# Kernel optimization log

Measured on AMD Instinct MI355X. Metric: run time of the kernel, lower is better.

The kernel has to match this reference:

```python
import jax, jax.numpy as jnp
import numpy as np

B, S, D, H = 4, 2048, 1024, 16
DH = D // H
NEG = -1.0e9


def setup_inputs() -> dict:
    key = jax.random.key(0)
    ks = jax.random.split(key, 12)
    sc = 1.0 / np.sqrt(D)
    inp = {
        'q': jax.random.normal(ks[0], (B, S, D), jnp.float32),
        'k': jax.random.normal(ks[1], (B, S, D), jnp.float32),
        'v': jax.random.normal(ks[2], (B, S, D), jnp.float32),
        # causal mask: 1.0 where attention is disallowed (strictly upper triangular)
        'mask': jnp.triu(jnp.ones((S, S), jnp.float32), k=1)[None, None, :, :],
        'Wq': jax.random.normal(ks[3], (D, D), jnp.float32) * sc,
        'bq': jnp.zeros((D,), jnp.float32),
        'Wk': jax.random.normal(ks[4], (D, D), jnp.float32) * sc,
        'bk': jnp.zeros((D,), jnp.float32),
        'Wv': jax.random.normal(ks[5], (D, D), jnp.float32) * sc,
        'bv': jnp.zeros((D,), jnp.float32),
        'Wo': jax.random.normal(ks[6], (D, D), jnp.float32) * sc,
        'bo': jnp.zeros((D,), jnp.float32),
    }
    return inp


def _split_heads(x):
    # [B,S,D] -> [B,H,S,DH]
    return x.reshape(B, S, H, DH).transpose(0, 2, 1, 3)


def reference(q, k, v, mask, Wq, bq, Wk, bk, Wv, bv, Wo, bo):
    _q = _split_heads(q @ Wq.T + bq)
    _k = _split_heads(k @ Wk.T + bk)
    _v = _split_heads(v @ Wv.T + bv)
    # faithful quirk: mask*-1e9 added BEFORE scaling, scale = sqrt(model_dim)
    score = jnp.einsum('bhqd,bhkd->bhqk', _q, _k) + mask * NEG
    attn = jax.nn.softmax(score / jnp.sqrt(jnp.float32(D)), axis=-1)
    ctx = jnp.einsum('bhqk,bhkd->bhqd', attn, _v)
    ctx = ctx.transpose(0, 2, 1, 3).reshape(B, S, D)
    return ctx @ Wo.T + bo
```

## Files before the change

### kernel.cpp

```cpp
#include <hip/hip_runtime.h>
#include <hip/hip_bf16.h>

#define S_ 2048
#define DH_ 64
#define NE_ 8388608

using f32x4  = __attribute__((ext_vector_type(4))) float;
using bf16x8 = __attribute__((ext_vector_type(8))) __bf16;
using bf16x4 = __attribute__((ext_vector_type(4))) __bf16;

__device__ __forceinline__ unsigned int f2bf(float f) {
    union { float f; unsigned int u; } x; x.f = f;
    return (x.u + 0x7FFFu + ((x.u >> 16) & 1u)) >> 16;
}

__device__ __forceinline__ void gl_lds16(const unsigned short* g, unsigned short* l) {
    __builtin_amdgcn_global_load_lds(
        (const __attribute__((address_space(1))) unsigned int*)(const void*)g,
        (__attribute__((address_space(3))) unsigned int*)(void*)l,
        16, 0, 0);
}

__global__ __launch_bounds__(256) void cvt_w4(const float* __restrict__ w0, const float* __restrict__ w1,
                                              const float* __restrict__ w2, const float* __restrict__ w3,
                                              unsigned short* __restrict__ out) {
    const float* src = blockIdx.y == 0 ? w0 : blockIdx.y == 1 ? w1 : blockIdx.y == 2 ? w2 : w3;
    unsigned short* dst = out + (size_t)blockIdx.y * 1048576;
    int i = (blockIdx.x * 256 + threadIdx.x) * 4;
    float4 v = *(const float4*)&src[i];
    ushort4 h;
    h.x = f2bf(v.x); h.y = f2bf(v.y); h.z = f2bf(v.z); h.w = f2bf(v.w);
    *(ushort4*)&dst[i] = h;
}

__global__ __launch_bounds__(256) void cvt_a3(const float* __restrict__ a0, const float* __restrict__ a1,
                                              const float* __restrict__ a2, unsigned short* __restrict__ out) {
    const float* src = blockIdx.y == 0 ? a0 : blockIdx.y == 1 ? a1 : a2;
    unsigned short* dst = out + (size_t)blockIdx.y * NE_;
    int i = (blockIdx.x * 256 + threadIdx.x) * 4;
    float4 v = *(const float4*)&src[i];
    ushort4 h;
    h.x = f2bf(v.x); h.y = f2bf(v.y); h.z = f2bf(v.z); h.w = f2bf(v.w);
    *(ushort4*)&dst[i] = h;
}

__global__ __launch_bounds__(256) void gemm_qkv(const unsigned short* __restrict__ actb,
                                                const unsigned short* __restrict__ Wcat,
                                                const float* __restrict__ bq,
                                                const float* __restrict__ bk,
                                                const float* __restrict__ bvv,
                                                unsigned short* __restrict__ Qp,
                                                unsigned short* __restrict__ Kp,
                                                unsigned short* __restrict__ VTp,
                                                float scq)
{
    constexpr int K = 1024, BK = 32;
    __shared__ unsigned short As[128 * BK];
    __shared__ unsigned short Bs[128 * BK];

    const int tid = threadIdx.x, lane = tid & 63, wid = tid >> 6;
    const int row0 = blockIdx.x * 128, col0 = blockIdx.y * 128;
    const int range = blockIdx.y >> 3;
    const unsigned short* A = actb + (size_t)range * NE_;
    const int wm = (wid >> 1) * 64, wn = (wid & 1) * 64;
    const int fr = lane & 15, fg = lane >> 4;

    f32x4 acc[4][4] = {};

    const int srow = wid * 16 + (lane >> 2);
    const int scol = (lane & 3) * 8;
    const size_t abase = (size_t)(row0 + srow) * K + scol;
    const size_t bbase = (size_t)(col0 + srow) * K + scol;
    unsigned short* lA0 = &As[srow * BK + scol];
    unsigned short* lA1 = &As[(srow + 64) * BK + scol];
    unsigned short* lB0 = &Bs[srow * BK + scol];
    unsigned short* lB1 = &Bs[(srow + 64) * BK + scol];

    for (int k0 = 0; k0 < K; k0 += BK) {
        gl_lds16(&A[abase + k0], lA0);
        gl_lds16(&A[abase + (size_t)64 * K + k0], lA1);
        gl_lds16(&Wcat[bbase + k0], lB0);
        gl_lds16(&Wcat[bbase + (size_t)64 * K + k0], lB1);
        __syncthreads();

        bf16x8 af[4], bfr[4];
        #pragma unroll
        for (int i = 0; i < 4; ++i) af[i] = *(const bf16x8*)&As[(wm + i * 16 + fr) * BK + fg * 8];
        #pragma unroll
        for (int i = 0; i < 4; ++i) bfr[i] = *(const bf16x8*)&Bs[(wn + i * 16 + fr) * BK + fg * 8];
        #pragma unroll
        for (int i = 0; i < 4; ++i)
            #pragma unroll
            for (int j = 0; j < 4; ++j)
                acc[i][j] = __builtin_amdgcn_mfma_f32_16x16x32_bf16(af[i], bfr[j], acc[i][j], 0, 0, 0);
        __syncthreads();
    }

    const float os = range == 0 ? scq : 1.0f;
    const float* bp = range == 0 ? bq : range == 1 ? bk : bvv;
    unsigned short* OP = range == 0 ? Qp : Kp;

    #pragma unroll
    for (int i = 0; i < 4; ++i) {
        #pragma unroll
        for (int j = 0; j < 4; ++j) {
            int colr = (col0 + wn + j * 16 + fr) & 1023;
            float bias = bp[colr];
            int h = colr >> 6, dh = colr & 63;
            if (range == 2) {
                int row = row0 + wm + i * 16 + fg * 4;
                int b = row >> 11, s = row & 2047;
                unsigned int w0 = f2bf(acc[i][j][0] + bias) | (f2bf(acc[i][j][1] + bias) << 16);
                unsigned int w1 = f2bf(acc[i][j][2] + bias) | (f2bf(acc[i][j][3] + bias) << 16);
                *(uint2*)&VTp[((size_t)((b << 4) + h) * 64 + dh) * 2048 + s] = make_uint2(w0, w1);
            } else {
                #pragma unroll
                for (int r = 0; r < 4; ++r) {
                    int row = row0 + wm + i * 16 + fg * 4 + r;
                    int b = row >> 11, s = row & 2047;
                    OP[((((b << 4) + h) * 2048 + s) << 6) + dh] =
                        (unsigned short)f2bf((acc[i][j][r] + bias) * os);
                }
            }
        }
    }
}

__global__ __launch_bounds__(256) void gemm_o(const unsigned short* __restrict__ A,
                                              const unsigned short* __restrict__ Bw,
                                              const float* __restrict__ bias,
                                              float* __restrict__ Cf)
{
    constexpr int K = 1024, BK = 32, N = 1024;
    __shared__ unsigned short As[128 * BK];
    __shared__ unsigned short Bs[128 * BK];

    const int tid = threadIdx.x, lane = tid & 63, wid = tid >> 6;
    const int row0 = blockIdx.x * 128, col0 = blockIdx.y * 128;
    const int wm = (wid >> 1) * 64, wn = (wid & 1) * 64;
    const int fr = lane & 15, fg = lane >> 4;

    f32x4 acc[4][4] = {};

    const int srow = wid * 16 + (lane >> 2);
    const int scol = (lane & 3) * 8;
    const size_t abase = (size_t)(row0 + srow) * K + scol;
    const size_t bbase = (size_t)(col0 + srow) * K + scol;
    unsigned short* lA0 = &As[srow * BK + scol];
    unsigned short* lA1 = &As[(srow + 64) * BK + scol];
    unsigned short* lB0 = &Bs[srow * BK + scol];
    unsigned short* lB1 = &Bs[(srow + 64) * BK + scol];

    for (int k0 = 0; k0 < K; k0 += BK) {
        gl_lds16(&A[abase + k0], lA0);
        gl_lds16(&A[abase + (size_t)64 * K + k0], lA1);
        gl_lds16(&Bw[bbase + k0], lB0);
        gl_lds16(&Bw[bbase + (size_t)64 * K + k0], lB1);
        __syncthreads();

        bf16x8 af[4], bfr[4];
        #pragma unroll
        for (int i = 0; i < 4; ++i) af[i] = *(const bf16x8*)&As[(wm + i * 16 + fr) * BK + fg * 8];
        #pragma unroll
        for (int i = 0; i < 4; ++i) bfr[i] = *(const bf16x8*)&Bs[(wn + i * 16 + fr) * BK + fg * 8];
        #pragma unroll
        for (int i = 0; i < 4; ++i)
            #pragma unroll
            for (int j = 0; j < 4; ++j)
                acc[i][j] = __builtin_amdgcn_mfma_f32_16x16x32_bf16(af[i], bfr[j], acc[i][j], 0, 0, 0);
        __syncthreads();
    }

    #pragma unroll
    for (int i = 0; i < 4; ++i) {
        #pragma unroll
        for (int j = 0; j < 4; ++j) {
            int col = col0 + wn + j * 16 + fr;
            float bv = bias[col];
            #pragma unroll
            for (int r = 0; r < 4; ++r) {
                int row = row0 + wm + i * 16 + fg * 4 + r;
                Cf[(size_t)row * N + col] = acc[i][j][r] + bv;
            }
        }
    }
}

__global__ __launch_bounds__(512, 4) void attn_fwd5(const unsigned short* __restrict__ Qp,
                                                    const unsigned short* __restrict__ Kp,
                                                    const unsigned short* __restrict__ VTg,
                                                    unsigned short* __restrict__ ctx)
{
    __shared__ unsigned short Ks[64][68];
    __shared__ unsigned short Vt[64][68];
    __shared__ unsigned short Ps[8][16][68];

    const int lin = blockIdx.x;
    const int xcd = lin & 7;
    const int w = lin >> 3;
    const int bh = xcd * 8 + (w & 7);
    const int j = 15 - (w >> 3);
    const int b = bh >> 4, h = bh & 15;
    const int tid = threadIdx.x, lane = tid & 63, wid = tid >> 6;
    const int fr = lane & 15, fg = lane >> 4;

    const unsigned short* Qh  = Qp  + (size_t)bh * (S_ * DH_);
    const unsigned short* Kh  = Kp  + (size_t)bh * (S_ * DH_);
    const unsigned short* VTh = VTg + (size_t)bh * (DH_ * S_);

    const int srow = tid >> 3;
    const int scol = (tid & 7) * 8;

    bf16x8 ones;
    #pragma unroll
    for (int i = 0; i < 8; ++i) ones[i] = (__bf16)1.0f;

    const int q0 = j * 128;
    const int ntiles = 2 * (j + 1);
    const int rbase = q0 + wid * 16;
    const int qg = rbase + fr;

    bf16x8 qf[2];
    #pragma unroll
    for (int ks = 0; ks < 2; ++ks)
        qf[ks] = *(const bf16x8*)&Qh[(size_t)qg * 64 + ks * 32 + 8 * fg];

    f32x4 oacc[4] = {};
    float m_run = -3.0e38f, l_run = 0.0f;

    int4 kreg = *(const int4*)&Kh[(size_t)srow * 64 + scol];
    int4 vreg = *(const int4*)&VTh[(size_t)srow * 2048 + scol];

    for (int kt = 0; kt < ntiles; ++kt) {
        const int kv0 = kt * 64;
        __syncthreads();
        *(int4*)&Ks[srow][scol] = kreg;
        *(int4*)&Vt[srow][scol] = vreg;
        if (kt + 1 < ntiles) {
            const int kv1 = kv0 + 64;
            kreg = *(const int4*)&Kh[(size_t)(kv1 + srow) * 64 + scol];
            vreg = *(const int4*)&VTh[(size_t)srow * 2048 + kv1 + scol];
        }
        __syncthreads();

        if (kv0 > rbase + 15) continue;

        f32x4 sacc[4] = {};
        #pragma unroll
        for (int nt = 0; nt < 4; ++nt)
            #pragma unroll
            for (int ks = 0; ks < 2; ++ks) {
                bf16x8 kf = *(const bf16x8*)&Ks[nt * 16 + fr][ks * 32 + 8 * fg];
                sacc[nt] = __builtin_amdgcn_mfma_f32_16x16x32_bf16(kf, qf[ks], sacc[nt], 0, 0, 0);
            }

        if (kv0 + 63 > rbase) {
            const int kbase = kv0 + fg * 4;
            #pragma unroll
            for (int nt = 0; nt < 4; ++nt)
                #pragma unroll
                for (int r = 0; r < 4; ++r)
                    if (kbase + nt * 16 + r > qg) sacc[nt][r] = -3.0e38f;
        }

        float vm = sacc[0][0];
        #pragma unroll
        for (int nt = 0; nt < 4; ++nt)
            #pragma unroll
            for (int r = 0; r < 4; ++r) vm = fmaxf(vm, sacc[nt][r]);
        vm = fmaxf(vm, __shfl_xor(vm, 16));
        vm = fmaxf(vm, __shfl_xor(vm, 32));

        if (!__all(vm - m_run <= 8.0f)) {
            const float mn = fmaxf(m_run, vm);
            const float alpha = exp2f(m_run - mn);
            m_run = mn;
            l_run *= alpha;
            #pragma unroll
            for (int dt = 0; dt < 4; ++dt)
                #pragma unroll
                for (int r = 0; r < 4; ++r) oacc[dt][r] *= alpha;
        }

        #pragma unroll
        for (int nt = 0; nt < 4; ++nt) {
            bf16x4 t;
            t[0] = (__bf16)exp2f(sacc[nt][0] - m_run);
            t[1] = (__bf16)exp2f(sacc[nt][1] - m_run);
            t[2] = (__bf16)exp2f(sacc[nt][2] - m_run);
            t[3] = (__bf16)exp2f(sacc[nt][3] - m_run);
            *(bf16x4*)&Ps[wid][fr][nt * 16 + fg * 4] = t;
        }
        asm volatile("s_waitcnt lgkmcnt(0)" ::: "memory");

        bf16x8 pb[2];
        #pragma unroll
        for (int ks = 0; ks < 2; ++ks)
            pb[ks] = *(const bf16x8*)&Ps[wid][fr][ks * 32 + 8 * fg];

        f32x4 racc = {};
        #pragma unroll
        for (int ks = 0; ks < 2; ++ks)
            racc = __builtin_amdgcn_mfma_f32_16x16x32_bf16(ones, pb[ks], racc, 0, 0, 0);
        #pragma unroll
        for (int dt = 0; dt < 4; ++dt)
            #pragma unroll
            for (int ks = 0; ks < 2; ++ks) {
                bf16x8 vf = *(const bf16x8*)&Vt[dt * 16 + fr][ks * 32 + 8 * fg];
                oacc[dt] = __builtin_amdgcn_mfma_f32_16x16x32_bf16(vf, pb[ks], oacc[dt], 0, 0, 0);
            }
        l_run += racc[0];
    }

    const float linv = 1.0f / l_run;
    unsigned short* cb = &ctx[(size_t)(b * 2048 + qg) * 1024 + h * 64];
    #pragma unroll
    for (int dt = 0; dt < 4; ++dt) {
        unsigned int w0 = f2bf(oacc[dt][0] * linv) | (f2bf(oacc[dt][1] * linv) << 16);
        unsigned int w1 = f2bf(oacc[dt][2] * linv) | (f2bf(oacc[dt][3] * linv) << 16);
        *(uint2*)&cb[dt * 16 + fg * 4] = make_uint2(w0, w1);
    }
}

extern "C" void kernel_launch(void* const* d_in, const int* in_sizes, int n_in,
                              void* d_out, int out_size, void* d_ws, size_t ws_size,
                              hipStream_t stream)
{
    const float* q  = (const float*)d_in[0];
    const float* k  = (const float*)d_in[1];
    const float* v  = (const float*)d_in[2];
    const float* Wq = (const float*)d_in[4];
    const float* bq = (const float*)d_in[5];
    const float* Wk = (const float*)d_in[6];
    const float* bk = (const float*)d_in[7];
    const float* Wv = (const float*)d_in[8];
    const float* bv = (const float*)d_in[9];
    const float* Wo = (const float*)d_in[10];
    const float* bo = (const float*)d_in[11];
    float* out = (float*)d_out;

    unsigned short* Wcat = (unsigned short*)d_ws;
    unsigned short* actb = Wcat + 4 * 1048576;
    unsigned short* Qp   = actb + 3 * (size_t)NE_;
    unsigned short* Kp   = Qp + NE_;
    unsigned short* VTp  = Kp + NE_;
    unsigned short* Ctx  = VTp + NE_;

    const float SCQ = 0.045084220027780106f;

    dim3 blk(256);
    cvt_w4<<<dim3(1024, 4), blk, 0, stream>>>(Wq, Wk, Wv, Wo, Wcat);
    cvt_a3<<<dim3(8192, 3), blk, 0, stream>>>(q, k, v, actb);

    gemm_qkv<<<dim3(64, 24), blk, 0, stream>>>(actb, Wcat, bq, bk, bv, Qp, Kp, VTp, SCQ);

    attn_fwd5<<<dim3(1024), dim3(512), 0, stream>>>(Qp, Kp, VTp, Ctx);

    gemm_o<<<dim3(64, 8), blk, 0, stream>>>(Ctx, Wcat + 3 * 1048576, bo, out);
}
```

Before: 203.0 us.

## Fuse fp32-to-bf16 activation conversion into QKV GEMM and double-buffer GEMM tiles

Drops the separate activation conversion kernel. The QKV GEMM now loads fp32 q/k/v directly into registers, converts them to bf16 and writes them into a double-buffered LDS tile, prefetching the next tile while the current one is multiplied. The output projection GEMM also gets double-buffered LDS with async global-to-LDS prefetch. This removes an extra read/write pass over the activations and one launch, and overlaps loads with MFMA. In exchange the fp32 A reads are re-done by each column block (8 per range), LDS use doubles, and register pressure rises.

Measured after the change: 209.1 us. +3.0%, slower.

```diff
diff --git a/kernel.cpp b/kernel.cpp
--- a/kernel.cpp
+++ b/kernel.cpp
@@ -33,35 +33,26 @@
     *(ushort4*)&dst[i] = h;
 }
 
-__global__ __launch_bounds__(256) void cvt_a3(const float* __restrict__ a0, const float* __restrict__ a1,
-                                              const float* __restrict__ a2, unsigned short* __restrict__ out) {
-    const float* src = blockIdx.y == 0 ? a0 : blockIdx.y == 1 ? a1 : a2;
-    unsigned short* dst = out + (size_t)blockIdx.y * NE_;
-    int i = (blockIdx.x * 256 + threadIdx.x) * 4;
-    float4 v = *(const float4*)&src[i];
-    ushort4 h;
-    h.x = f2bf(v.x); h.y = f2bf(v.y); h.z = f2bf(v.z); h.w = f2bf(v.w);
-    *(ushort4*)&dst[i] = h;
-}
-
-__global__ __launch_bounds__(256) void gemm_qkv(const unsigned short* __restrict__ actb,
-                                                const unsigned short* __restrict__ Wcat,
-                                                const float* __restrict__ bq,
-                                                const float* __restrict__ bk,
-                                                const float* __restrict__ bvv,
-                                                unsigned short* __restrict__ Qp,
-                                                unsigned short* __restrict__ Kp,
-                                                unsigned short* __restrict__ VTp,
-                                                float scq)
+__global__ __launch_bounds__(256) void gemm_qkv_f(const float* __restrict__ qf32,
+                                                  const float* __restrict__ kf32,
+                                                  const float* __restrict__ vf32,
+                                                  const unsigned short* __restrict__ Wcat,
+                                                  const float* __restrict__ bq,
+                                                  const float* __restrict__ bk,
+                                                  const float* __restrict__ bvv,
+                                                  unsigned short* __restrict__ Qp,
+                                                  unsigned short* __restrict__ Kp,
+                                                  unsigned short* __restrict__ VTp,
+                                                  float scq)
 {
-    constexpr int K = 1024, BK = 32;
-    __shared__ unsigned short As[128 * BK];
-    __shared__ unsigned short Bs[128 * BK];
+    constexpr int K = 1024, BK = 32, NT = K / BK;
+    __shared__ unsigned short As[2][128 * BK];
+    __shared__ unsigned short Bs[2][128 * BK];
 
     const int tid = threadIdx.x, lane = tid & 63, wid = tid >> 6;
     const int row0 = blockIdx.x * 128, col0 = blockIdx.y * 128;
     const int range = blockIdx.y >> 3;
-    const unsigned short* A = actb + (size_t)range * NE_;
+    const float* A = range == 0 ? qf32 : range == 1 ? kf32 : vf32;
     const int wm = (wid >> 1) * 64, wn = (wid & 1) * 64;
     const int fr = lane & 15, fg = lane >> 4;
 
@@ -69,30 +60,61 @@
 
     const int srow = wid * 16 + (lane >> 2);
     const int scol = (lane & 3) * 8;
-    const size_t abase = (size_t)(row0 + srow) * K + scol;
     const size_t bbase = (size_t)(col0 + srow) * K + scol;
-    unsigned short* lA0 = &As[srow * BK + scol];
-    unsigned short* lA1 = &As[(srow + 64) * BK + scol];
-    unsigned short* lB0 = &Bs[srow * BK + scol];
-    unsigned short* lB1 = &Bs[(srow + 64) * BK + scol];
-
-    for (int k0 = 0; k0 < K; k0 += BK) {
-        gl_lds16(&A[abase + k0], lA0);
-        gl_lds16(&A[abase + (size_t)64 * K + k0], lA1);
-        gl_lds16(&Wcat[bbase + k0], lB0);
-        gl_lds16(&Wcat[bbase + (size_t)64 * K + k0], lB1);
-        __syncthreads();
+
+    const int arow = tid >> 1;
+    const int acol = (tid & 1) * 16;
+    const float* agp = A + (size_t)(row0 + arow) * K + acol;
+
+    float4 ar[4];
+    #pragma unroll
+    for (int u = 0; u < 4; ++u) ar[u] = *(const float4*)&agp[4 * u];
+
+    gl_lds16(&Wcat[bbase], &Bs[0][srow * BK + scol]);
+    gl_lds16(&Wcat[bbase + (size_t)64 * K], &Bs[0][(srow + 64) * BK + scol]);
+
+    {
+        bf16x8 h0, h1;
+        h0[0] = (__bf16)ar[0].x; h0[1] = (__bf16)ar[0].y; h0[2] = (__bf16)ar[0].z; h0[3] = (__bf16)ar[0].w;
+        h0[4] = (__bf16)ar[1].x; h0[5] = (__bf16)ar[1].y; h0[6] = (__bf16)ar[1].z; h0[7] = (__bf16)ar[1].w;
+        h1[0] = (__bf16)ar[2].x; h1[1] = (__bf16)ar[2].y; h1[2] = (__bf16)ar[2].z; h1[3] = (__bf16)ar[2].w;
+        h1[4] = (__bf16)ar[3].x; h1[5] = (__bf16)ar[3].y; h1[6] = (__bf16)ar[3].z; h1[7] = (__bf16)ar[3].w;
+        *(bf16x8*)&As[0][arow * BK + acol] = h0;
+        *(bf16x8*)&As[0][arow * BK + acol + 8] = h1;
+    }
+    __syncthreads();
+
+    for (int t = 0; t < NT; ++t) {
+        const int cur = t & 1;
+        const bool more = (t + 1 < NT);
+        if (more) {
+            const int k1 = (t + 1) * BK;
+            #pragma unroll
+            for (int u = 0; u < 4; ++u) ar[u] = *(const float4*)&agp[k1 + 4 * u];
+            gl_lds16(&Wcat[bbase + k1], &Bs[cur ^ 1][srow * BK + scol]);
+            gl_lds16(&Wcat[bbase + (size_t)64 * K + k1], &Bs[cur ^ 1][(srow + 64) * BK + scol]);
+        }
 
         bf16x8 af[4], bfr[4];
         #pragma unroll
-        for (int i = 0; i < 4; ++i) af[i] = *(const bf16x8*)&As[(wm + i * 16 + fr) * BK + fg * 8];
-        #pragma unroll
-        for (int i = 0; i < 4; ++i) bfr[i] = *(const bf16x8*)&Bs[(wn + i * 16 + fr) * BK + fg * 8];
+        for (int i = 0; i < 4; ++i) af[i] = *(const bf16x8*)&As[cur][(wm + i * 16 + fr) * BK + fg * 8];
+        #pragma unroll
+        for (int i = 0; i < 4; ++i) bfr[i] = *(const bf16x8*)&Bs[cur][(wn + i * 16 + fr) * BK + fg * 8];
         #pragma unroll
         for (int i = 0; i < 4; ++i)
             #pragma unroll
             for (int j = 0; j < 4; ++j)
                 acc[i][j] = __builtin_amdgcn_mfma_f32_16x16x32_bf16(af[i], bfr[j], acc[i][j], 0, 0, 0);
+
+        if (more) {
+            bf16x8 h0, h1;
+            h0[0] = (__bf16)ar[0].x; h0[1] = (__bf16)ar[0].y; h0[2] = (__bf16)ar[0].z; h0[3] = (__bf16)ar[0].w;
+            h0[4] = (__bf16)ar[1].x; h0[5] = (__bf16)ar[1].y; h0[6] = (__bf16)ar[1].z; h0[7] = (__bf16)ar[1].w;
+            h1[0] = (__bf16)ar[2].x; h1[1] = (__bf16)ar[2].y; h1[2] = (__bf16)ar[2].z; h1[3] = (__bf16)ar[2].w;
+            h1[4] = (__bf16)ar[3].x; h1[5] = (__bf16)ar[3].y; h1[6] = (__bf16)ar[3].z; h1[7] = (__bf16)ar[3].w;
+            *(bf16x8*)&As[cur ^ 1][arow * BK + acol] = h0;
+            *(bf16x8*)&As[cur ^ 1][arow * BK + acol + 8] = h1;
+        }
         __syncthreads();
     }
 
@@ -131,9 +153,9 @@
                                               const float* __restrict__ bias,
                                               float* __restrict__ Cf)
 {
-    constexpr int K = 1024, BK = 32, N = 1024;
-    __shared__ unsigned short As[128 * BK];
-    __shared__ unsigned short Bs[128 * BK];
+    constexpr int K = 1024, BK = 32, N = 1024, NT = K / BK;
+    __shared__ unsigned short As[2][128 * BK];
+    __shared__ unsigned short Bs[2][128 * BK];
 
     const int tid = threadIdx.x, lane = tid & 63, wid = tid >> 6;
     const int row0 = blockIdx.x * 128, col0 = blockIdx.y * 128;
@@ -146,23 +168,28 @@
     const int scol = (lane & 3) * 8;
     const size_t abase = (size_t)(row0 + srow) * K + scol;
     const size_t bbase = (size_t)(col0 + srow) * K + scol;
-    unsigned short* lA0 = &As[srow * BK + scol];
-    unsigned short* lA1 = &As[(srow + 64) * BK + scol];
-    unsigned short* lB0 = &Bs[srow * BK + scol];
-    unsigned short* lB1 = &Bs[(srow + 64) * BK + scol];
-
-    for (int k0 = 0; k0 < K; k0 += BK) {
-        gl_lds16(&A[abase + k0], lA0);
-        gl_lds16(&A[abase + (size_t)64 * K + k0], lA1);
-        gl_lds16(&Bw[bbase + k0], lB0);
-        gl_lds16(&Bw[bbase + (size_t)64 * K + k0], lB1);
-        __syncthreads();
+
+    gl_lds16(&A[abase], &As[0][srow * BK + scol]);
+    gl_lds16(&A[abase + (size_t)64 * K], &As[0][(srow + 64) * BK + scol]);
+    gl_lds16(&Bw[bbase], &Bs[0][srow * BK + scol]);
+    gl_lds16(&Bw[bbase + (size_t)64 * K], &Bs[0][(srow + 64) * BK + scol]);
+    __syncthreads();
+
+    for (int t = 0; t < NT; ++t) {
+        const int cur = t & 1;
+        if (t + 1 < NT) {
+            const int k1 = (t + 1) * BK;
+            gl_lds16(&A[abase + k1], &As[cur ^ 1][srow * BK + scol]);
+            gl_lds16(&A[abase + (size_t)64 * K + k1], &As[cur ^ 1][(srow + 64) * BK + scol]);
+            gl_lds16(&Bw[bbase + k1], &Bs[cur ^ 1][srow * BK + scol]);
+            gl_lds16(&Bw[bbase + (size_t)64 * K + k1], &Bs[cur ^ 1][(srow + 64) * BK + scol]);
+        }
 
         bf16x8 af[4], bfr[4];
         #pragma unroll
-        for (int i = 0; i < 4; ++i) af[i] = *(const bf16x8*)&As[(wm + i * 16 + fr) * BK + fg * 8];
-        #pragma unroll
-        for (int i = 0; i < 4; ++i) bfr[i] = *(const bf16x8*)&Bs[(wn + i * 16 + fr) * BK + fg * 8];
+        for (int i = 0; i < 4; ++i) af[i] = *(const bf16x8*)&As[cur][(wm + i * 16 + fr) * BK + fg * 8];
+        #pragma unroll
+        for (int i = 0; i < 4; ++i) bfr[i] = *(const bf16x8*)&Bs[cur][(wn + i * 16 + fr) * BK + fg * 8];
         #pragma unroll
         for (int i = 0; i < 4; ++i)
             #pragma unroll
@@ -340,8 +367,7 @@
     float* out = (float*)d_out;
 
     unsigned short* Wcat = (unsigned short*)d_ws;
-    unsigned short* actb = Wcat + 4 * 1048576;
-    unsigned short* Qp   = actb + 3 * (size_t)NE_;
+    unsigned short* Qp   = Wcat + 4 * 1048576;
     unsigned short* Kp   = Qp + NE_;
     unsigned short* VTp  = Kp + NE_;
     unsigned short* Ctx  = VTp + NE_;
@@ -350,9 +376,8 @@
 
     dim3 blk(256);
     cvt_w4<<<dim3(1024, 4), blk, 0, stream>>>(Wq, Wk, Wv, Wo, Wcat);
-    cvt_a3<<<dim3(8192, 3), blk, 0, stream>>>(q, k, v, actb);
-
-    gemm_qkv<<<dim3(64, 24), blk, 0, stream>>>(actb, Wcat, bq, bk, bv, Qp, Kp, VTp, SCQ);
+
+    gemm_qkv_f<<<dim3(64, 24), blk, 0, stream>>>(q, k, v, Wcat, bq, bk, bv, Qp, Kp, VTp, SCQ);
 
     attn_fwd5<<<dim3(1024), dim3(512), 0, stream>>>(Qp, Kp, VTp, Ctx);
 
```

## Rewrite QKV projection GEMM with 256x256 tiles, double-buffered LDS and swizzle

Applied to the files above, without the earlier changes.

Replaces the 128x128, 4-wave QKV GEMM with a 256x256-tile, 8-wave kernel that uses BK=64 and double-buffers A and B in LDS. Async global-to-LDS copies for the next k-tile are interleaved with the MFMA phases, using explicit waitcnt, barriers and setprio. An XOR swizzle is applied to LDS addresses, and blocks are remapped across XCDs so neighbouring tiles share cache. The aim is to raise arithmetic intensity and overlap memory latency with compute. The cost is 128 KB of LDS per block, more registers, and only 384 blocks, which lowers occupancy and parallelism.

Result: no change. 205.4 us (+1.2%).

```diff
diff --git a/kernel.cpp b/kernel.cpp
--- a/kernel.cpp
+++ b/kernel.cpp
@@ -44,71 +44,117 @@
     *(ushort4*)&dst[i] = h;
 }
 
-__global__ __launch_bounds__(256) void gemm_qkv(const unsigned short* __restrict__ actb,
-                                                const unsigned short* __restrict__ Wcat,
-                                                const float* __restrict__ bq,
-                                                const float* __restrict__ bk,
-                                                const float* __restrict__ bvv,
-                                                unsigned short* __restrict__ Qp,
-                                                unsigned short* __restrict__ Kp,
-                                                unsigned short* __restrict__ VTp,
-                                                float scq)
+__global__ __launch_bounds__(512, 2) void gemm_qkv8(const unsigned short* __restrict__ actb,
+                                                    const unsigned short* __restrict__ Wcat,
+                                                    const float* __restrict__ bq,
+                                                    const float* __restrict__ bk,
+                                                    const float* __restrict__ bvv,
+                                                    unsigned short* __restrict__ Qp,
+                                                    unsigned short* __restrict__ Kp,
+                                                    unsigned short* __restrict__ VTp,
+                                                    float scq)
 {
-    constexpr int K = 1024, BK = 32;
-    __shared__ unsigned short As[128 * BK];
-    __shared__ unsigned short Bs[128 * BK];
+    __shared__ unsigned short lds[65536];
+    unsigned short* ldsA = lds;
+    unsigned short* ldsB = lds + 32768;
+
+    const int orig = blockIdx.x;
+    const int lid = (orig & 7) * 48 + (orig >> 3);
+    const int bx = lid & 31;
+    const int by = lid >> 5;
+    const int range = by >> 2;
+    const unsigned short* Aact = actb + (size_t)range * NE_;
 
     const int tid = threadIdx.x, lane = tid & 63, wid = tid >> 6;
-    const int row0 = blockIdx.x * 128, col0 = blockIdx.y * 128;
-    const int range = blockIdx.y >> 3;
-    const unsigned short* A = actb + (size_t)range * NE_;
-    const int wm = (wid >> 1) * 64, wn = (wid & 1) * 64;
     const int fr = lane & 15, fg = lane >> 4;
-
-    f32x4 acc[4][4] = {};
-
-    const int srow = wid * 16 + (lane >> 2);
-    const int scol = (lane & 3) * 8;
-    const size_t abase = (size_t)(row0 + srow) * K + scol;
-    const size_t bbase = (size_t)(col0 + srow) * K + scol;
-    unsigned short* lA0 = &As[srow * BK + scol];
-    unsigned short* lA1 = &As[(srow + 64) * BK + scol];
-    unsigned short* lB0 = &Bs[srow * BK + scol];
-    unsigned short* lB1 = &Bs[(srow + 64) * BK + scol];
-
-    for (int k0 = 0; k0 < K; k0 += BK) {
-        gl_lds16(&A[abase + k0], lA0);
-        gl_lds16(&A[abase + (size_t)64 * K + k0], lA1);
-        gl_lds16(&Wcat[bbase + k0], lB0);
-        gl_lds16(&Wcat[bbase + (size_t)64 * K + k0], lB1);
-        __syncthreads();
-
-        bf16x8 af[4], bfr[4];
-        #pragma unroll
-        for (int i = 0; i < 4; ++i) af[i] = *(const bf16x8*)&As[(wm + i * 16 + fr) * BK + fg * 8];
-        #pragma unroll
-        for (int i = 0; i < 4; ++i) bfr[i] = *(const bf16x8*)&Bs[(wn + i * 16 + fr) * BK + fg * 8];
-        #pragma unroll
-        for (int i = 0; i < 4; ++i)
-            #pragma unroll
-            for (int j = 0; j < 4; ++j)
-                acc[i][j] = __builtin_amdgcn_mfma_f32_16x16x32_bf16(af[i], bfr[j], acc[i][j], 0, 0, 0);
-        __syncthreads();
-    }
-
+    const int wid_m = wid >> 2, wid_n = wid & 3;
+
+    const int srcRow0 = wid * 16 + (lane >> 3);
+    const int scolS = ((((lane & 7) * 16) ^ (lane & 32)) >> 1);
+
+    auto STG = [&](int ldsRegion, const unsigned short* g, int grow, int kk) {
+        const unsigned short* s0 = g + (size_t)(grow + srcRow0) * 1024 + kk + scolS;
+        gl_lds16(s0, lds + ldsRegion + wid * 1024 + lane * 8);
+        gl_lds16(s0 + 8 * 1024, lds + ldsRegion + wid * 1024 + 512 + lane * 8);
+    };
+
+    const int flipR = (fr & 4) ? 16 : 0;
+    const int vA = wid_m * 8192 + fr * 64 + ((fg * 8) ^ flipR);
+    const int vB = (wid_n & 1) * 4096 + fr * 64 + ((fg * 8) ^ flipR) + (wid_n >> 1) * 8192;
+
+    f32x4 acc[8][4] = {};
+    bf16x8 bfr[4][2];
+
+    STG(0,          Aact, bx * 256,       0);
+    STG(8192,       Aact, bx * 256 + 128, 0);
+    STG(32768,      Wcat, by * 256,       0);
+    STG(32768+8192, Wcat, by * 256 + 128, 0);
+    STG(32768+16384,       Wcat, by * 256,       64);
+    STG(32768+16384+8192,  Wcat, by * 256 + 128,  64);
+    asm volatile("s_waitcnt vmcnt(4)" ::: "memory");
+    __builtin_amdgcn_s_barrier();
+
+#define KTILE(BUF, ABUF, TA, BBUF, TB)                                              \
+  {                                                                                 \
+    _Pragma("unroll")                                                               \
+    for (int q = 0; q < 4; ++q) {                                                   \
+      if (q == 0) {                                                                 \
+        _Pragma("unroll")                                                           \
+        for (int j = 0; j < 4; ++j) {                                               \
+          bfr[j][0] = *(const bf16x8*)&ldsB[(BUF)*16384 + vB + j*1024];             \
+          bfr[j][1] = *(const bf16x8*)&ldsB[(BUF)*16384 + vB + j*1024 + 32];        \
+        }                                                                           \
+      }                                                                             \
+      bf16x8 af[2][2];                                                              \
+      _Pragma("unroll")                                                             \
+      for (int i2 = 0; i2 < 2; ++i2) {                                              \
+        af[i2][0] = *(const bf16x8*)&ldsA[(BUF)*16384 + vA + (q*2+i2)*1024];        \
+        af[i2][1] = *(const bf16x8*)&ldsA[(BUF)*16384 + vA + (q*2+i2)*1024 + 32];   \
+      }                                                                             \
+      if (q == 0) STG((ABUF)*16384,        Aact, bx*256,       ((TA)&15)*64);       \
+      if (q == 1) STG((ABUF)*16384 + 8192, Aact, bx*256 + 128, ((TA)&15)*64);       \
+      if (q == 2) STG(32768 + (BBUF)*16384,        Wcat, by*256,       ((TB)&15)*64); \
+      if (q == 3) { STG(32768 + (BBUF)*16384 + 8192, Wcat, by*256 + 128, ((TB)&15)*64); \
+                    asm volatile("s_waitcnt vmcnt(4)" ::: "memory"); }              \
+      __builtin_amdgcn_s_barrier();                                                 \
+      asm volatile("s_waitcnt lgkmcnt(0)" ::: "memory");                            \
+      __builtin_amdgcn_s_setprio(1);                                                \
+      _Pragma("unroll")                                                             \
+      for (int i2 = 0; i2 < 2; ++i2)                                                \
+        _Pragma("unroll")                                                           \
+        for (int j = 0; j < 4; ++j) {                                               \
+          acc[q*2+i2][j] = __builtin_amdgcn_mfma_f32_16x16x32_bf16(af[i2][0], bfr[j][0], acc[q*2+i2][j], 0, 0, 0); \
+          acc[q*2+i2][j] = __builtin_amdgcn_mfma_f32_16x16x32_bf16(af[i2][1], bfr[j][1], acc[q*2+i2][j], 0, 0, 0); \
+        }                                                                           \
+      __builtin_amdgcn_s_setprio(0);                                                \
+      __builtin_amdgcn_s_barrier();                                                 \
+    }                                                                               \
+  }
+
+    for (int it = 0; it < 8; ++it) {
+        const int t0 = 2 * it;
+        KTILE(0, 1, t0 + 1, 0, t0 + 2);
+        KTILE(1, 0, t0 + 2, 1, t0 + 3);
+    }
+#undef KTILE
+
+    asm volatile("s_waitcnt vmcnt(0)" ::: "memory");
+
+    const float* bp = range == 0 ? bq : range == 1 ? bk : bvv;
     const float os = range == 0 ? scq : 1.0f;
-    const float* bp = range == 0 ? bq : range == 1 ? bk : bvv;
     unsigned short* OP = range == 0 ? Qp : Kp;
+    const int row00 = bx * 256 + wid_m * 128;
+    const int col0r = (by & 3) * 256 + wid_n * 64;
 
     #pragma unroll
-    for (int i = 0; i < 4; ++i) {
+    for (int i = 0; i < 8; ++i) {
         #pragma unroll
         for (int j = 0; j < 4; ++j) {
-            int colr = (col0 + wn + j * 16 + fr) & 1023;
+            int colr = col0r + j * 16 + fr;
             float bias = bp[colr];
             int h = colr >> 6, dh = colr & 63;
             if (range == 2) {
-                int row = row0 + wm + i * 16 + fg * 4;
+                int row = row00 + i * 16 + fg * 4;
                 int b = row >> 11, s = row & 2047;
                 unsigned int w0 = f2bf(acc[i][j][0] + bias) | (f2bf(acc[i][j][1] + bias) << 16);
                 unsigned int w1 = f2bf(acc[i][j][2] + bias) | (f2bf(acc[i][j][3] + bias) << 16);
@@ -116,7 +162,7 @@
             } else {
                 #pragma unroll
                 for (int r = 0; r < 4; ++r) {
-                    int row = row0 + wm + i * 16 + fg * 4 + r;
+                    int row = row00 + i * 16 + fg * 4 + r;
                     int b = row >> 11, s = row & 2047;
                     OP[((((b << 4) + h) * 2048 + s) << 6) + dh] =
                         (unsigned short)f2bf((acc[i][j][r] + bias) * os);
@@ -352,7 +398,7 @@
     cvt_w4<<<dim3(1024, 4), blk, 0, stream>>>(Wq, Wk, Wv, Wo, Wcat);
     cvt_a3<<<dim3(8192, 3), blk, 0, stream>>>(q, k, v, actb);
 
-    gemm_qkv<<<dim3(64, 24), blk, 0, stream>>>(actb, Wcat, bq, bk, bv, Qp, Kp, VTp, SCQ);
+    gemm_qkv8<<<dim3(384), dim3(512), 0, stream>>>(actb, Wcat, bq, bk, bv, Qp, Kp, VTp, SCQ);
 
     attn_fwd5<<<dim3(1024), dim3(512), 0, stream>>>(Qp, Kp, VTp, Ctx);
 
```
